# Kernel optimization log

Hardware: AMD Instinct MI355X
Metric: run time of the kernel (lower is better)

The kernel has to match this reference:

```python
import jax, jax.numpy as jnp
import numpy as np

B, C, IC, W, H, Z = 2, 128, 64, 32, 32, 128  # sub_sample=True -> new_z = Z//2
BN_EPS = 1e-5


def setup_inputs() -> dict:
    key = jax.random.key(0)
    ks = jax.random.split(key, 14)
    n = lambda k, shape, sc=1.0: jax.random.normal(k, shape, jnp.float32) * sc
    return {
        "x": n(ks[0], (B, C, W, H, Z)),
        "g_w": n(ks[1], (IC, C), 0.05), "g_b": n(ks[2], (IC,), 0.05),
        "theta_w": n(ks[3], (IC, C), 0.05), "theta_b": n(ks[4], (IC,), 0.05),
        "phi_w": n(ks[5], (IC, C), 0.05), "phi_b": n(ks[6], (IC,), 0.05),
        "cat_w": n(ks[7], (2 * IC,), 0.1),           # Conv2d(2*IC -> 1, 1x1, bias=False)
        "W_w": n(ks[8], (C, IC), 0.05), "W_b": n(ks[9], (C,), 0.05),
        "bn_g": n(ks[10], (C,), 0.1), "bn_b": n(ks[11], (C,), 0.1),
        "bn_m": n(ks[12], (C,), 0.1),
        "bn_v": jax.random.uniform(ks[13], (C,), jnp.float32, 0.5, 1.5),
    }


def _conv1x1(x, w, b):
    # 1x1x1 Conv3d == per-voxel channel matmul. x: (b,c,w,h,z), w: (o,c)
    y = jnp.einsum('bcwhz,oc->bowhz', x, w)
    return y + b[None, :, None, None, None]


def _pool_z(t):
    # MaxPool3d(kernel=(1,1,2)): halve last dim by pairwise max
    return t.reshape(*t.shape[:-1], t.shape[-1] // 2, 2).max(-1)


def reference(x, g_w, g_b, theta_w, theta_b, phi_w, phi_b, cat_w,
              W_w, W_b, bn_g, bn_b, bn_m, bn_v):
    b, c, w, h, z = x.shape
    ic = g_w.shape[0]
    nz = z // 2  # sub_sample

    g_x = _pool_z(_conv1x1(x, g_w, g_b))                     # (b, ic, w, h, nz)
    g_x = g_x.transpose(0, 2, 3, 4, 1).reshape(-1, nz, ic)    # (n, nz, ic), n=b*w*h

    theta = _conv1x1(x, theta_w, theta_b)                     # (b, ic, w, h, z)
    theta = theta.transpose(0, 2, 3, 1, 4).reshape(-1, ic, z)  # (n, ic, z)
    phi = _pool_z(_conv1x1(x, phi_w, phi_b))                  # (b, ic, w, h, nz)
    phi = phi.transpose(0, 2, 3, 1, 4).reshape(-1, ic, nz)     # (n, ic, nz)

    # concat + 1x1 Conv2d(2ic->1) + ReLU == relu(w_t . theta_i + w_p . phi_j)
    a = jnp.einsum('nci,c->ni', theta, cat_w[:ic])             # (n, z)
    bb = jnp.einsum('ncj,c->nj', phi, cat_w[ic:])              # (n, nz)
    f = jax.nn.relu(a[:, :, None] + bb[:, None, :]) / nz       # (n, z, nz), /N norm

    y = jnp.einsum('nij,njc->nic', f, g_x)                     # (n, z, ic)
    y = y.reshape(b, w, h, z, ic).transpose(0, 4, 1, 2, 3)      # (b, ic, w, h, z)

    Wy = _conv1x1(y, W_w, W_b)                                 # (b, c, w, h, z)
    scale = (bn_g / jnp.sqrt(bn_v + BN_EPS))[None, :, None, None, None]
    Wy = (Wy - bn_m[None, :, None, None, None]) * scale + bn_b[None, :, None, None, None]
    return Wy + x
```

## Files before the change

### kernel.cpp

```cpp
#include <hip/hip_runtime.h>
#include <hip/hip_bf16.h>


#define C_      128
#define IC_     64
#define Z_      128
#define NZ_     64
#define CSTRIDE 131072
#define NPIX    2048
#define PPB     4
#define YSTRIDE 68

typedef __attribute__((ext_vector_type(8))) short short8;
typedef __attribute__((ext_vector_type(4))) float f32x4;

union S8 { short8 s; uint4 u4; uint2 u2[2]; unsigned short h[8]; };

__device__ __forceinline__ unsigned short f2b(float f) {
    union { __hip_bfloat16 h; unsigned short u; } cv;
    cv.h = __float2bfloat16(f);
    return cv.u;
}

__device__ __forceinline__ void gl16(const float* g, float* l) {
    __builtin_amdgcn_global_load_lds(
        (const __attribute__((address_space(1))) void*)g,
        (__attribute__((address_space(3))) void*)l, 16, 0, 0);
}

__global__ void nlb_prep(
    const float* __restrict__ g_w,   const float* __restrict__ theta_w,
    const float* __restrict__ phi_w, const float* __restrict__ W_w,
    const float* __restrict__ g_b,   const float* __restrict__ theta_b,
    const float* __restrict__ phi_b, const float* __restrict__ cat_w,
    const float* __restrict__ W_b,   const float* __restrict__ bn_g,
    const float* __restrict__ bn_b,  const float* __restrict__ bn_m,
    const float* __restrict__ bn_v,
    unsigned short* __restrict__ wcat, unsigned short* __restrict__ Wwb,
    float* __restrict__ twp, float* __restrict__ alphap, float* __restrict__ betap,
    float* __restrict__ cbp, float* __restrict__ cw2p, float* __restrict__ tbp)
{
    const int t = threadIdx.x;
    for (int idx = t; idx < 128 * 128; idx += 256) {
        const int oc = idx >> 7, c = idx & 127;
        const float v = (oc < 64) ? g_w[oc * 128 + c] : phi_w[(oc - 64) * 128 + c];
        wcat[idx] = f2b(v);
    }
    for (int idx = t; idx < 128 * 64; idx += 256)
        Wwb[idx] = f2b(W_w[idx]);
    if (t < 128) {
        float s = 0.f;
        for (int oc = 0; oc < 64; ++oc) s += cat_w[oc] * theta_w[oc * 128 + t];
        twp[t] = s;
        const float sc = bn_g[t] * rsqrtf(bn_v[t] + 1e-5f);
        alphap[t] = sc;
        betap[t]  = (W_b[t] - bn_m[t]) * sc + bn_b[t];
        cbp[t] = (t < 64) ? g_b[t] : phi_b[t - 64];
    }
    if (t < 64) cw2p[t] = cat_w[64 + t];
    if (t == 0) {
        float s = 0.f;
        for (int oc = 0; oc < 64; ++oc) s += cat_w[oc] * theta_b[oc];
        tbp[0] = s;
    }
}

__global__ __launch_bounds__(256, 2) void nlb_main(
    const float* __restrict__ x,
    const unsigned short* __restrict__ wcat,
    const unsigned short* __restrict__ Wwb,
    const float* __restrict__ twp, const float* __restrict__ alphap,
    const float* __restrict__ betap, const float* __restrict__ cbp,
    const float* __restrict__ cw2p, const float* __restrict__ tbp,
    float* __restrict__ out)
{
    const int tid  = threadIdx.x;
    const int lane = tid & 63;
    const int wv   = tid >> 6;
    const int n16  = lane & 15;
    const int q    = lane >> 4;
    const int pix0 = blockIdx.x * PPB;

    __shared__ float xs0[8192];
    __shared__ float xs1[8192];
    __shared__ unsigned short gp[64 * 72];
    __shared__ float a_s[128], b_s[64];
    __shared__ float alpha_s[128], beta_s[128], cb_s[128], cw2_s[64];
    __shared__ unsigned short twb_s[128];
    unsigned short* ys = (unsigned short*)xs1;

    auto PBASE = [&](int pix) -> size_t {
        const int b  = pix >> 10;
        const int wh = pix & 1023;
        return (size_t)b * C_ * CSTRIDE + (size_t)wh * Z_;
    };

    auto STAGE_ISSUE = [&](size_t gbase, int h, float* dst) {
        #pragma unroll
        for (int it = 0; it < 8; ++it) {
            const int idx = it * 256 + tid;
            const int c = idx >> 4, zq = idx & 15;
            const float* g = &x[gbase + (size_t)c * CSTRIDE + h * 64 + zq * 4];
            float* l = dst + it * 1024 + wv * 256;
            gl16(g, l);
        }
    };

    const float tb = tbp[0];

    auto PHASEA = [&](int h, const float* xsrc) {
        const int zl = 16 * wv + n16;
        short8 af[4];
        #pragma unroll
        for (int kt = 0; kt < 4; ++kt) {
            const int c0 = kt * 32 + q * 8;
            S8 t;
            #pragma unroll
            for (int e = 0; e < 8; ++e) t.h[e] = f2b(xsrc[(c0 + e) * 64 + zl]);
            af[kt] = t.s;
        }
        {
            f32x4 acc = {tb, tb, tb, tb};
            #pragma unroll
            for (int kt = 0; kt < 4; ++kt) {
                S8 bfa;
                bfa.u4 = (n16 == 0) ? *(const uint4*)&twb_s[kt * 32 + q * 8]
                                    : (uint4){0u, 0u, 0u, 0u};
                acc = __builtin_amdgcn_mfma_f32_16x16x32_bf16(af[kt], bfa.s, acc, 0, 0, 0);
            }
            if (n16 == 0) {
                #pragma unroll
                for (int r = 0; r < 4; ++r)
                    a_s[h * 64 + 16 * wv + q * 4 + r] = acc[r];
            }
        }
        float bsum0 = 0.f, bsum1 = 0.f;
        const int j0 = h * 32 + 8 * wv + 2 * q;
        #pragma unroll
        for (int oct = 0; oct < 8; ++oct) {
            const int oc = oct * 16 + n16;
            const float bias = cb_s[oc];
            f32x4 acc = {bias, bias, bias, bias};
            const unsigned short* wrow = wcat + oc * 128;
            #pragma unroll
            for (int k = 0; k < 4; ++k) {
                const short8 bf = *(const short8*)&wrow[k * 32 + q * 8];
                acc = __builtin_amdgcn_mfma_f32_16x16x32_bf16(af[k], bf, acc, 0, 0, 0);
            }
            const float p0 = fmaxf(acc[0], acc[1]);
            const float p1 = fmaxf(acc[2], acc[3]);
            if (oct < 4) {
                gp[oc * 72 + j0]     = f2b(p0);
                gp[oc * 72 + j0 + 1] = f2b(p1);
            } else {
                const float cw = cw2_s[oc - 64];
                bsum0 += cw * p0; bsum1 += cw * p1;
            }
        }
        #pragma unroll
        for (int m = 1; m < 16; m <<= 1) {
            bsum0 += __shfl_xor(bsum0, m);
            bsum1 += __shfl_xor(bsum1, m);
        }
        if (n16 == 0) b_s[j0]     = bsum0;
        if (n16 == 1) b_s[j0 + 1] = bsum1;
    };

    STAGE_ISSUE(PBASE(pix0), 0, xs0);
    STAGE_ISSUE(PBASE(pix0), 1, xs1);
    if (tid < 128) {
        alpha_s[tid] = alphap[tid]; beta_s[tid] = betap[tid];
        twb_s[tid] = f2b(twp[tid]); cb_s[tid] = cbp[tid];
    }
    if (tid < 64) cw2_s[tid] = cw2p[tid];

    for (int pp = 0; pp < PPB; ++pp) {
        const size_t base = PBASE(pix0 + pp);
        const bool pf = (pp + 1 < PPB);

        asm volatile("s_waitcnt vmcnt(8) lgkmcnt(0)" ::: "memory");
        __builtin_amdgcn_s_barrier();
        PHASEA(0, xs0);
        asm volatile("s_waitcnt lgkmcnt(0)" ::: "memory");
        __builtin_amdgcn_s_barrier();
        if (pf) STAGE_ISSUE(PBASE(pix0 + pp + 1), 0, xs0);
        if (pf) { asm volatile("s_waitcnt vmcnt(8) lgkmcnt(0)" ::: "memory"); }
        else    { asm volatile("s_waitcnt vmcnt(0) lgkmcnt(0)" ::: "memory"); }
        __builtin_amdgcn_s_barrier();
        PHASEA(1, xs1);
        asm volatile("s_waitcnt lgkmcnt(0)" ::: "memory");
        __builtin_amdgcn_s_barrier();

        {
            const int i0 = 32 * wv;
            short8 bfrag[4][2];
            #pragma unroll
            for (int nt = 0; nt < 4; ++nt)
                #pragma unroll
                for (int k = 0; k < 2; ++k)
                    bfrag[nt][k] = *(const short8*)&gp[(nt * 16 + n16) * 72 + k * 32 + q * 8];
            float bv[2][8];
            #pragma unroll
            for (int k = 0; k < 2; ++k)
                #pragma unroll
                for (int jj = 0; jj < 8; ++jj)
                    bv[k][jj] = b_s[k * 32 + q * 8 + jj];
            f32x4 acc[2][4];
            #pragma unroll
            for (int mt = 0; mt < 2; ++mt) {
                const float ai = a_s[i0 + mt * 16 + n16];
                #pragma unroll
                for (int nt = 0; nt < 4; ++nt) acc[mt][nt] = (f32x4){0.f, 0.f, 0.f, 0.f};
                #pragma unroll
                for (int k = 0; k < 2; ++k) {
                    S8 fr;
                    #pragma unroll
                    for (int jj = 0; jj < 8; ++jj)
                        fr.h[jj] = f2b(fmaxf(ai + bv[k][jj], 0.f) * 0.015625f);
                    #pragma unroll
                    for (int nt = 0; nt < 4; ++nt)
                        acc[mt][nt] = __builtin_amdgcn_mfma_f32_16x16x32_bf16(
                            fr.s, bfrag[nt][k], acc[mt][nt], 0, 0, 0);
                }
            }
            #pragma unroll
            for (int mt = 0; mt < 2; ++mt)
                #pragma unroll
                for (int nt = 0; nt < 4; ++nt)
                    #pragma unroll
                    for (int r = 0; r < 4; ++r) {
                        const int i  = i0 + mt * 16 + q * 4 + r;
                        const int oc = nt * 16 + n16;
                        ys[i * YSTRIDE + oc] = f2b(acc[mt][nt][r]);
                    }
        }
        asm volatile("s_waitcnt lgkmcnt(0)" ::: "memory");
        __builtin_amdgcn_s_barrier();

        {
            const int zt0 = 2 * wv;
            short8 bC[2][2];
            #pragma unroll
            for (int zt = 0; zt < 2; ++zt)
                #pragma unroll
                for (int k = 0; k < 2; ++k) {
                    const int z = (zt0 + zt) * 16 + n16;
                    S8 t;
                    t.u2[0] = *(const uint2*)&ys[z * YSTRIDE + k * 32 + q * 8];
                    t.u2[1] = *(const uint2*)&ys[z * YSTRIDE + k * 32 + q * 8 + 4];
                    bC[zt][k] = t.s;
                }
            #pragma unroll
            for (int mt = 0; mt < 8; ++mt) {
                short8 aC[2];
                const int ca = mt * 16 + n16;
                #pragma unroll
                for (int k = 0; k < 2; ++k)
                    aC[k] = *(const short8*)&Wwb[ca * 64 + k * 32 + q * 8];
                float al[4], be[4];
                #pragma unroll
                for (int r = 0; r < 4; ++r) {
                    const int cr = mt * 16 + q * 4 + r;
                    al[r] = alpha_s[cr]; be[r] = beta_s[cr];
                }
                #pragma unroll
                for (int zt = 0; zt < 2; ++zt) {
                    f32x4 acc = {0.f, 0.f, 0.f, 0.f};
                    #pragma unroll
                    for (int k = 0; k < 2; ++k)
                        acc = __builtin_amdgcn_mfma_f32_16x16x32_bf16(aC[k], bC[zt][k], acc, 0, 0, 0);
                    const int z = (zt0 + zt) * 16 + n16;
                    #pragma unroll
                    for (int r = 0; r < 4; ++r) {
                        const int cr = mt * 16 + q * 4 + r;
                        const size_t gaddr = base + (size_t)cr * CSTRIDE + z;
                        out[gaddr] = acc[r] * al[r] + be[r] + x[gaddr];
                    }
                }
            }
        }
        asm volatile("s_waitcnt lgkmcnt(0)" ::: "memory");
        __builtin_amdgcn_s_barrier();
        if (pf) STAGE_ISSUE(PBASE(pix0 + pp + 1), 1, xs1);
    }
}

extern "C" void kernel_launch(void* const* d_in, const int* in_sizes, int n_in,
                              void* d_out, int out_size, void* d_ws, size_t ws_size,
                              hipStream_t stream) {
    const float* x       = (const float*)d_in[0];
    const float* g_w     = (const float*)d_in[1];
    const float* g_b     = (const float*)d_in[2];
    const float* theta_w = (const float*)d_in[3];
    const float* theta_b = (const float*)d_in[4];
    const float* phi_w   = (const float*)d_in[5];
    const float* phi_b   = (const float*)d_in[6];
    const float* cat_w   = (const float*)d_in[7];
    const float* W_w     = (const float*)d_in[8];
    const float* W_b     = (const float*)d_in[9];
    const float* bn_g    = (const float*)d_in[10];
    const float* bn_b    = (const float*)d_in[11];
    const float* bn_m    = (const float*)d_in[12];
    const float* bn_v    = (const float*)d_in[13];
    float* out = (float*)d_out;

    char* ws = (char*)d_ws;
    unsigned short* wcat = (unsigned short*)ws;
    unsigned short* Wwb  = (unsigned short*)(ws + 32768);
    float* twp    = (float*)(ws + 49152);
    float* alphap = (float*)(ws + 49664);
    float* betap  = (float*)(ws + 50176);
    float* cbp    = (float*)(ws + 50688);
    float* cw2p   = (float*)(ws + 51200);
    float* tbp    = (float*)(ws + 51456);

    nlb_prep<<<dim3(1), dim3(256), 0, stream>>>(
        g_w, theta_w, phi_w, W_w, g_b, theta_b, phi_b, cat_w, W_b,
        bn_g, bn_b, bn_m, bn_v,
        wcat, Wwb, twp, alphap, betap, cbp, cw2p, tbp);

    nlb_main<<<dim3(NPIX / PPB), dim3(256), 0, stream>>>(
        x, wcat, Wwb, twp, alphap, betap, cbp, cw2p, tbp, out);
}
```

Before: 350.8 us.

## Stream x in channel quarters through 4-slot LDS ring and raise occupancy

Replaces the two full half-pixel x staging buffers with a 4-slot ring of 32-channel quarter tiles. The next quarter is issued three steps ahead, and phase A accumulates the projection MFMAs incrementally over the quarters. LDS use shrinks (xs 32KB, and gp and ys share one union buffer), pixels per block drop to 2, and launch bounds ask for 3 blocks per CU. The LDS tiles also get an XOR swizzle to cut bank conflicts. The trade-off is more barriers per pixel, a shallower prefetch distance, and twice as many blocks.

Measured after the change: 540.9 us. 1.54x slower.

```diff
diff --git a/kernel.cpp b/kernel.cpp
--- a/kernel.cpp
+++ b/kernel.cpp
@@ -8,7 +8,8 @@
 #define NZ_     64
 #define CSTRIDE 131072
 #define NPIX    2048
-#define PPB     4
+#define PPB     2
+#define NQ      (PPB * 8)
 #define YSTRIDE 68
 
 typedef __attribute__((ext_vector_type(8))) short short8;
@@ -27,6 +28,10 @@
         (const __attribute__((address_space(1))) void*)g,
         (__attribute__((address_space(3))) void*)l, 16, 0, 0);
 }
+
+#define WAITV4() asm volatile("s_waitcnt vmcnt(4)" ::: "memory")
+#define BARL()   do { asm volatile("s_waitcnt lgkmcnt(0)" ::: "memory"); \
+                      __builtin_amdgcn_s_barrier(); } while (0)
 
 __global__ void nlb_prep(
     const float* __restrict__ g_w,   const float* __restrict__ theta_w,
@@ -65,7 +70,7 @@
     }
 }
 
-__global__ __launch_bounds__(256, 2) void nlb_main(
+__global__ __launch_bounds__(256, 3) void nlb_main(
     const float* __restrict__ x,
     const unsigned short* __restrict__ wcat,
     const unsigned short* __restrict__ Wwb,
@@ -81,13 +86,11 @@
     const int q    = lane >> 4;
     const int pix0 = blockIdx.x * PPB;
 
-    __shared__ float xs0[8192];
-    __shared__ float xs1[8192];
-    __shared__ unsigned short gp[64 * 72];
+    __shared__ float xs[4 * 2048];
+    __shared__ unsigned short un[128 * YSTRIDE];
     __shared__ float a_s[128], b_s[64];
     __shared__ float alpha_s[128], beta_s[128], cb_s[128], cw2_s[64];
     __shared__ unsigned short twb_s[128];
-    unsigned short* ys = (unsigned short*)xs1;
 
     auto PBASE = [&](int pix) -> size_t {
         const int b  = pix >> 10;
@@ -95,63 +98,71 @@
         return (size_t)b * C_ * CSTRIDE + (size_t)wh * Z_;
     };
 
-    auto STAGE_ISSUE = [&](size_t gbase, int h, float* dst) {
-        #pragma unroll
-        for (int it = 0; it < 8; ++it) {
+    auto ISSUE_Q = [&](int s) {
+        if (s >= NQ) return;
+        const size_t gbase = PBASE(pix0 + (s >> 3));
+        const int h = (s >> 2) & 1, kt = s & 3, slot = s & 3;
+        #pragma unroll
+        for (int it = 0; it < 2; ++it) {
             const int idx = it * 256 + tid;
-            const int c = idx >> 4, zq = idx & 15;
-            const float* g = &x[gbase + (size_t)c * CSTRIDE + h * 64 + zq * 4];
-            float* l = dst + it * 1024 + wv * 256;
+            const int cl = idx >> 4, zq = idx & 15;
+            const int zsw = (zq * 4) ^ (((cl >> 3) & 1) << 4);
+            const float* g = &x[gbase + (size_t)(kt * 32 + cl) * CSTRIDE + h * 64 + zsw];
+            float* l = xs + slot * 2048 + it * 1024 + wv * 256;
             gl16(g, l);
         }
     };
 
     const float tb = tbp[0];
 
-    auto PHASEA = [&](int h, const float* xsrc) {
+    auto PHASEA = [&](int h, int qbase) {
         const int zl = 16 * wv + n16;
-        short8 af[4];
+        const int zz = zl ^ ((q & 1) << 4);
+        f32x4 acc[8];
+        #pragma unroll
+        for (int oct = 0; oct < 8; ++oct) {
+            const float bias = cb_s[oct * 16 + n16];
+            acc[oct] = (f32x4){bias, bias, bias, bias};
+        }
+        f32x4 aacc = {tb, tb, tb, tb};
         #pragma unroll
         for (int kt = 0; kt < 4; ++kt) {
-            const int c0 = kt * 32 + q * 8;
+            const int s = qbase + kt;
+            WAITV4();
+            BARL();
+            ISSUE_Q(s + 3);
+            const float* xsrc = xs + (s & 3) * 2048;
             S8 t;
-            #pragma unroll
-            for (int e = 0; e < 8; ++e) t.h[e] = f2b(xsrc[(c0 + e) * 64 + zl]);
-            af[kt] = t.s;
-        }
-        {
-            f32x4 acc = {tb, tb, tb, tb};
-            #pragma unroll
-            for (int kt = 0; kt < 4; ++kt) {
-                S8 bfa;
-                bfa.u4 = (n16 == 0) ? *(const uint4*)&twb_s[kt * 32 + q * 8]
-                                    : (uint4){0u, 0u, 0u, 0u};
-                acc = __builtin_amdgcn_mfma_f32_16x16x32_bf16(af[kt], bfa.s, acc, 0, 0, 0);
+            const int cl0 = q * 8;
+            #pragma unroll
+            for (int e = 0; e < 8; ++e)
+                t.h[e] = f2b(xsrc[(cl0 + e) * 64 + zz]);
+            const short8 af = t.s;
+            S8 bfa;
+            bfa.u4 = (n16 == 0) ? *(const uint4*)&twb_s[kt * 32 + q * 8]
+                                : (uint4){0u, 0u, 0u, 0u};
+            aacc = __builtin_amdgcn_mfma_f32_16x16x32_bf16(af, bfa.s, aacc, 0, 0, 0);
+            #pragma unroll
+            for (int oct = 0; oct < 8; ++oct) {
+                const short8 bf = *(const short8*)&wcat[(oct * 16 + n16) * 128 + kt * 32 + q * 8];
+                acc[oct] = __builtin_amdgcn_mfma_f32_16x16x32_bf16(af, bf, acc[oct], 0, 0, 0);
             }
-            if (n16 == 0) {
-                #pragma unroll
-                for (int r = 0; r < 4; ++r)
-                    a_s[h * 64 + 16 * wv + q * 4 + r] = acc[r];
-            }
+        }
+        if (n16 == 0) {
+            #pragma unroll
+            for (int r = 0; r < 4; ++r)
+                a_s[h * 64 + 16 * wv + q * 4 + r] = aacc[r];
         }
         float bsum0 = 0.f, bsum1 = 0.f;
         const int j0 = h * 32 + 8 * wv + 2 * q;
         #pragma unroll
         for (int oct = 0; oct < 8; ++oct) {
+            const float p0 = fmaxf(acc[oct][0], acc[oct][1]);
+            const float p1 = fmaxf(acc[oct][2], acc[oct][3]);
             const int oc = oct * 16 + n16;
-            const float bias = cb_s[oc];
-            f32x4 acc = {bias, bias, bias, bias};
-            const unsigned short* wrow = wcat + oc * 128;
-            #pragma unroll
-            for (int k = 0; k < 4; ++k) {
-                const short8 bf = *(const short8*)&wrow[k * 32 + q * 8];
-                acc = __builtin_amdgcn_mfma_f32_16x16x32_bf16(af[k], bf, acc, 0, 0, 0);
-            }
-            const float p0 = fmaxf(acc[0], acc[1]);
-            const float p1 = fmaxf(acc[2], acc[3]);
             if (oct < 4) {
-                gp[oc * 72 + j0]     = f2b(p0);
-                gp[oc * 72 + j0 + 1] = f2b(p1);
+                un[oc * 72 + j0]     = f2b(p0);
+                un[oc * 72 + j0 + 1] = f2b(p1);
             } else {
                 const float cw = cw2_s[oc - 64];
                 bsum0 += cw * p0; bsum1 += cw * p1;
@@ -166,8 +177,7 @@
         if (n16 == 1) b_s[j0 + 1] = bsum1;
     };
 
-    STAGE_ISSUE(PBASE(pix0), 0, xs0);
-    STAGE_ISSUE(PBASE(pix0), 1, xs1);
+    ISSUE_Q(0); ISSUE_Q(1); ISSUE_Q(2);
     if (tid < 128) {
         alpha_s[tid] = alphap[tid]; beta_s[tid] = betap[tid];
         twb_s[tid] = f2b(twp[tid]); cb_s[tid] = cbp[tid];
@@ -176,20 +186,10 @@
 
     for (int pp = 0; pp < PPB; ++pp) {
         const size_t base = PBASE(pix0 + pp);
-        const bool pf = (pp + 1 < PPB);
-
-        asm volatile("s_waitcnt vmcnt(8) lgkmcnt(0)" ::: "memory");
-        __builtin_amdgcn_s_barrier();
-        PHASEA(0, xs0);
-        asm volatile("s_waitcnt lgkmcnt(0)" ::: "memory");
-        __builtin_amdgcn_s_barrier();
-        if (pf) STAGE_ISSUE(PBASE(pix0 + pp + 1), 0, xs0);
-        if (pf) { asm volatile("s_waitcnt vmcnt(8) lgkmcnt(0)" ::: "memory"); }
-        else    { asm volatile("s_waitcnt vmcnt(0) lgkmcnt(0)" ::: "memory"); }
-        __builtin_amdgcn_s_barrier();
-        PHASEA(1, xs1);
-        asm volatile("s_waitcnt lgkmcnt(0)" ::: "memory");
-        __builtin_amdgcn_s_barrier();
+
+        PHASEA(0, pp * 8);
+        PHASEA(1, pp * 8 + 4);
+        BARL();
 
         {
             const int i0 = 32 * wv;
@@ -198,17 +198,20 @@
             for (int nt = 0; nt < 4; ++nt)
                 #pragma unroll
                 for (int k = 0; k < 2; ++k)
-                    bfrag[nt][k] = *(const short8*)&gp[(nt * 16 + n16) * 72 + k * 32 + q * 8];
+                    bfrag[nt][k] = *(const short8*)&un[(nt * 16 + n16) * 72 + k * 32 + q * 8];
             float bv[2][8];
             #pragma unroll
             for (int k = 0; k < 2; ++k)
                 #pragma unroll
                 for (int jj = 0; jj < 8; ++jj)
                     bv[k][jj] = b_s[k * 32 + q * 8 + jj];
+            float ai[2];
+            #pragma unroll
+            for (int mt = 0; mt < 2; ++mt) ai[mt] = a_s[i0 + mt * 16 + n16];
+            BARL();
             f32x4 acc[2][4];
             #pragma unroll
             for (int mt = 0; mt < 2; ++mt) {
-                const float ai = a_s[i0 + mt * 16 + n16];
                 #pragma unroll
                 for (int nt = 0; nt < 4; ++nt) acc[mt][nt] = (f32x4){0.f, 0.f, 0.f, 0.f};
                 #pragma unroll
@@ -216,7 +219,7 @@
                     S8 fr;
                     #pragma unroll
                     for (int jj = 0; jj < 8; ++jj)
-                        fr.h[jj] = f2b(fmaxf(ai + bv[k][jj], 0.f) * 0.015625f);
+                        fr.h[jj] = f2b(fmaxf(ai[mt] + bv[k][jj], 0.f) * 0.015625f);
                     #pragma unroll
                     for (int nt = 0; nt < 4; ++nt)
                         acc[mt][nt] = __builtin_amdgcn_mfma_f32_16x16x32_bf16(
@@ -231,11 +234,10 @@
                     for (int r = 0; r < 4; ++r) {
                         const int i  = i0 + mt * 16 + q * 4 + r;
                         const int oc = nt * 16 + n16;
-                        ys[i * YSTRIDE + oc] = f2b(acc[mt][nt][r]);
+                        un[i * YSTRIDE + oc] = f2b(acc[mt][nt][r]);
                     }
         }
-        asm volatile("s_waitcnt lgkmcnt(0)" ::: "memory");
-        __builtin_amdgcn_s_barrier();
+        BARL();
 
         {
             const int zt0 = 2 * wv;
@@ -246,8 +248,8 @@
                 for (int k = 0; k < 2; ++k) {
                     const int z = (zt0 + zt) * 16 + n16;
                     S8 t;
-                    t.u2[0] = *(const uint2*)&ys[z * YSTRIDE + k * 32 + q * 8];
-                    t.u2[1] = *(const uint2*)&ys[z * YSTRIDE + k * 32 + q * 8 + 4];
+                    t.u2[0] = *(const uint2*)&un[z * YSTRIDE + k * 32 + q * 8];
+                    t.u2[1] = *(const uint2*)&un[z * YSTRIDE + k * 32 + q * 8 + 4];
                     bC[zt][k] = t.s;
                 }
             #pragma unroll
@@ -279,9 +281,6 @@
                 }
             }
         }
-        asm volatile("s_waitcnt lgkmcnt(0)" ::: "memory");
-        __builtin_amdgcn_s_barrier();
-        if (pf) STAGE_ISSUE(PBASE(pix0 + pp + 1), 1, xs1);
     }
 }
 
```
